# Kernel tuning notes

Measured on AMD Instinct MI355X. Metric: run time of the kernel, lower is better.

## Reference

```python
import jax, jax.numpy as jnp
import numpy as np

BS, OBS_LEN, TS, GW, GH = 1024, 8, 64, 32, 32
HID = 64          # hidden size of both LSTMs (hardcoded in __init__)
TEOM_IN = 36      # 6*6 flattened teom features (zeros in the original forward)


def setup_inputs() -> dict:
    key = jax.random.key(0)
    ks = jax.random.split(key, 22)
    r = lambda k, s, sc=0.1: jax.random.normal(k, s, dtype=jnp.float32) * sc
    return dict(
        obsv=r(ks[0], (BS, OBS_LEN, 2), 1.0),
        teom=jax.random.uniform(ks[1], (BS, TS, GW, GH), dtype=jnp.float32),
        # lstm_obsv (input 2 -> hidden 64), PyTorch gate order i,f,g,o
        Wih_o=r(ks[2], (4 * HID, 2)), Whh_o=r(ks[3], (4 * HID, HID)),
        bih_o=r(ks[4], (4 * HID,)), bhh_o=r(ks[5], (4 * HID,)),
        # lstm_teom (input 36 -> hidden 64)
        Wih_t=r(ks[6], (4 * HID, TEOM_IN)), Whh_t=r(ks[7], (4 * HID, HID)),
        bih_t=r(ks[8], (4 * HID,)), bhh_t=r(ks[9], (4 * HID,)),
        Wof=r(ks[10], (64, HID)), bof=r(ks[11], (64,)),
        Wtf=r(ks[12], (64, HID)), btf=r(ks[13], (64,)),
        Wmix=r(ks[14], (64, 128)), bmix=r(ks[15], (64,)),
        W1=r(ks[16], (32, 64)), b1=r(ks[17], (32,)),
        W2=r(ks[18], (32, 32)), b2=r(ks[19], (32,)),
        W3=r(ks[20], (2, 32)), b3=r(ks[21], (2,)),
    )


def _cell(x, h, c, Wih, Whh, b):
    # standard torch LSTMCell math; b = b_ih + b_hh
    g = x @ Wih.T + h @ Whh.T + b
    i, f, gg, o = jnp.split(g, 4, axis=-1)
    c_new = jax.nn.sigmoid(f) * c + jax.nn.sigmoid(i) * jnp.tanh(gg)
    h_new = jax.nn.sigmoid(o) * jnp.tanh(c_new)
    return h_new, c_new


def reference(obsv, teom, Wih_o, Whh_o, bih_o, bhh_o, Wih_t, Whh_t, bih_t, bhh_t,
              Wof, bof, Wtf, btf, Wmix, bmix, W1, b1, W2, b2, W3, b3):
    bs, out_len = teom.shape[0], teom.shape[1]
    dt = obsv.dtype
    b_o = bih_o + bhh_o
    b_t = bih_t + bhh_t
    # conved_teom_flat is hard zeros in the original forward (convs never called)
    z_teom = jnp.zeros((bs, Wih_t.shape[1]), dt)
    lrelu = lambda v: jnp.where(v >= 0, v, 0.1 * v)  # LeakyReLU(0.1)

    def mix_out(h_t, h_o, buf):
        # buf: [bs, 3, 2] = last three positions (obsv[:,-3:,:])
        ts_ = h_t @ Wtf.T + btf
        os_ = h_o @ Wof.T + bof
        m = jnp.concatenate([ts_, os_], axis=1) @ Wmix.T + bmix
        a = lrelu(m @ W1.T + b1)
        a = lrelu(a @ W2.T + b2)
        o = a @ W3.T + b3
        # y = out(y_mix) + obsv[:,-1,:] + (obsv[:,-1,:] - obsv[:,-3,:]) / 2
        return o + buf[:, -1] + (buf[:, -1] - buf[:, 0]) * 0.5

    h_o = jnp.zeros((bs, HID), dt); c_o = jnp.zeros((bs, HID), dt)
    h_t = jnp.zeros((bs, HID), dt); c_t = jnp.zeros((bs, HID), dt)

    # ---- t == 0: obsv LSTM consumes the full observed trajectory
    def obsv_scan(carry, x_t):
        h, c = carry
        h, c = _cell(x_t, h, c, Wih_o, Whh_o, b_o)
        return (h, c), None
    (h_o, c_o), _ = jax.lax.scan(obsv_scan, (h_o, c_o), obsv.transpose(1, 0, 2))
    h_t, c_t = _cell(z_teom, h_t, c_t, Wih_t, Whh_t, b_t)
    buf = obsv[:, -3:, :]
    y0 = mix_out(h_t, h_o, buf)
    buf = jnp.concatenate([buf[:, 1:], y0[:, None]], axis=1)

    # ---- t = 1 .. out_len-1: obsv LSTM steps on previous prediction
    def step(carry, _):
        h_o, c_o, h_t, c_t, buf = carry
        h_t, c_t = _cell(z_teom, h_t, c_t, Wih_t, Whh_t, b_t)
        h_o, c_o = _cell(buf[:, -1], h_o, c_o, Wih_o, Whh_o, b_o)
        y_t = mix_out(h_t, h_o, buf)
        buf = jnp.concatenate([buf[:, 1:], y_t[:, None]], axis=1)
        return (h_o, c_o, h_t, c_t, buf), y_t

    _, ys = jax.lax.scan(step, (h_o, c_o, h_t, c_t, buf), None, length=out_len - 1)
    y = jnp.concatenate([y0[:, None], ys.transpose(1, 0, 2)], axis=1)  # [bs, out_len, 2]
    # teom_cropped is all-zeros in the original forward -> c is exactly zeros
    c_out = jnp.zeros((bs, out_len), dt)
    return y, c_out
```

## Files before the change

### kernel.cpp

```cpp
#include <hip/hip_runtime.h>

#define BS 1024
#define TS 64

__device__ __forceinline__ float sigf(float x){ return 1.f/(1.f+__expf(-x)); }
__device__ __forceinline__ float tanh_fast(float x){
  float cx = fminf(fmaxf(x,-15.f),15.f);
  float e = __expf(2.f*cx);
  return (e-1.f)/(e+1.f);
}
__device__ __forceinline__ float lrelu(float v){ return v>=0.f ? v : 0.1f*v; }
__device__ __forceinline__ float dot4(float4 a, float4 b){
  return a.x*b.x + a.y*b.y + a.z*b.z + a.w*b.w;
}

__global__ __launch_bounds__(256) void precompute_kernel(
    const float* __restrict__ Whh_t, const float* __restrict__ bih_t,
    const float* __restrict__ bhh_t,
    const float* __restrict__ Wof,  const float* __restrict__ bof,
    const float* __restrict__ Wtf,  const float* __restrict__ btf,
    const float* __restrict__ Wmix, const float* __restrict__ bmix,
    float* __restrict__ ws_wcomb, float* __restrict__ ws_mbias)
{
  __shared__ __align__(16) float sHall[TS*64];
  __shared__ __align__(16) float sTs[TS*64];
  __shared__ float sWof[64*64];
  __shared__ float sG[256];
  __shared__ float sBof[64];
  __shared__ float sCmr[64];

  const int t = threadIdx.x;

  float4 wrow[16];
#pragma unroll
  for (int j=0;j<16;++j) wrow[j] = reinterpret_cast<const float4*>(Whh_t + t*64)[j];
  const float btr = bih_t[t] + bhh_t[t];

  for (int i=t;i<4096;i+=256) sWof[i] = Wof[i];
  if (t<64) sBof[t] = bof[t];
  __syncthreads();

  float c_reg = 0.f;
  for (int s=0;s<TS;++s){
    float a0=btr, a1=0.f, a2=0.f, a3=0.f;
    if (s>0){
      const float4* h4 = reinterpret_cast<const float4*>(sHall + (s-1)*64);
#pragma unroll
      for (int j=0;j<16;j+=4){
        a0 += dot4(wrow[j],   h4[j]);
        a1 += dot4(wrow[j+1], h4[j+1]);
        a2 += dot4(wrow[j+2], h4[j+2]);
        a3 += dot4(wrow[j+3], h4[j+3]);
      }
    }
    sG[t] = (a0+a1)+(a2+a3);
    __syncthreads();
    if (t<64){
      float gi=sG[t], gf=sG[64+t], gg=sG[128+t], go=sG[192+t];
      c_reg = sigf(gf)*c_reg + sigf(gi)*tanh_fast(gg);
      sHall[s*64+t] = sigf(go)*tanh_fast(c_reg);
    }
    __syncthreads();
  }

  if (t<64){
    float acc = bmix[t];
    for (int k=0;k<64;++k) acc += Wmix[t*128+64+k]*sBof[k];
    sCmr[t] = acc;
  }
  for (int o=t;o<TS*64;o+=256){
    int s=o>>6, i=o&63;
    float acc = btf[i];
    for (int k=0;k<64;++k) acc += Wtf[i*64+k]*sHall[s*64+k];
    sTs[o] = acc;
  }
  for (int o=t;o<4096;o+=256){
    int r=o>>6, j=o&63;
    float acc = 0.f;
    for (int k=0;k<64;++k) acc += Wmix[r*128+64+k]*sWof[k*64+j];
    ws_wcomb[o] = acc;
  }
  __syncthreads();
  for (int o=t;o<TS*64;o+=256){
    int s=o>>6, j=o&63;
    float acc = sCmr[j];
    for (int k=0;k<64;++k) acc += Wmix[j*128+k]*sTs[s*64+k];
    ws_mbias[o] = acc;
  }
}

__global__ __launch_bounds__(256, 4) void main_kernel(
    const float* __restrict__ obsv,
    const float* __restrict__ Wih_o, const float* __restrict__ Whh_o,
    const float* __restrict__ bih_o, const float* __restrict__ bhh_o,
    const float* __restrict__ W1, const float* __restrict__ b1,
    const float* __restrict__ W2, const float* __restrict__ b2,
    const float* __restrict__ W3, const float* __restrict__ b3,
    const float* __restrict__ wcomb, const float* __restrict__ mbias,
    float* __restrict__ out)
{
  __shared__ __align__(16) float4 sWc[16*64];
  __shared__ __align__(16) float4 sW1[16*32];
  __shared__ __align__(16) float4 sW2[8*32];
  __shared__ float sG[256];
  __shared__ __align__(16) float sHb[64];
  __shared__ __align__(16) float sM[64];
  __shared__ __align__(16) float sA1[32];
  __shared__ float sY[2];
  __shared__ float sObs[16];

  const int t    = threadIdx.x;
  const int blk  = blockIdx.x;
  const int lane = t & 63;
  const int w    = t >> 6;
  const int tw   = (blk + (blk >> 8)) & 3;
  const bool tailw = (w == tw);

  if (t < 64) out[BS*TS*2 + blk*64 + t] = 0.f;

  for (int i=t;i<1024;i+=256) sWc[i] = reinterpret_cast<const float4*>(wcomb)[(i&63)*16 + (i>>6)];
  for (int i=t;i<512;i+=256)  sW1[i] = reinterpret_cast<const float4*>(W1)[(i&31)*16 + (i>>5)];
  if (t<256)                  sW2[t] = reinterpret_cast<const float4*>(W2)[(t&31)*8 + (t>>5)];
  if (t<16) sObs[t] = obsv[blk*16 + t];
  if (t<64) sHb[t] = 0.f;

  float4 wrow[16];
#pragma unroll
  for (int j=0;j<16;++j) wrow[j] = reinterpret_cast<const float4*>(Whh_o + t*64)[j];
  const float wi0  = Wih_o[2*t];
  const float wi1  = Wih_o[2*t+1];
  const float b_or = bih_o[t] + bhh_o[t];

  const int rr = lane & 31, hf = lane >> 5;
  const float b1r = b1[rr], b2r = b2[rr];
  const float w30 = W3[rr], w31 = W3[32+rr];
  const float b30 = b3[0],  b31 = b3[1];
  float bl00=0,bl01=0,bl10=0,bl11=0,bl20=0,bl21=0;
  float c_reg = 0.f;

  __syncthreads();

  if (tailw){
    bl00 = sObs[10]; bl01 = sObs[11];
    bl10 = sObs[12]; bl11 = sObs[13];
    bl20 = sObs[14]; bl21 = sObs[15];
  }

  const float4* sH4   = reinterpret_cast<const float4*>(sHb);
  const float4* sM4   = reinterpret_cast<const float4*>(sM);
  const float4* sA14  = reinterpret_cast<const float4*>(sA1);

  for (int it=0; it<71; ++it){
    float mb = 0.f;
    if (tailw && it >= 7) mb = mbias[(it-7)*64 + lane];

    float x0, x1;
    if (it < 8){ x0 = sObs[2*it]; x1 = sObs[2*it+1]; }
    else       { x0 = sY[0];      x1 = sY[1]; }
    float a0 = b_or + wi0*x0 + wi1*x1, p0 = 0.f;
#pragma unroll
    for (int q=0;q<16;q+=2){
      a0 += dot4(wrow[q],   sH4[q]);
      p0 += dot4(wrow[q+1], sH4[q+1]);
    }
    sG[t] = a0 + p0;
    __syncthreads();

    if (tailw){
      __builtin_amdgcn_s_setprio(1);
      const float g0 = sG[lane],     g1 = sG[64+lane];
      const float g2 = sG[128+lane], g3 = sG[192+lane];
      c_reg = sigf(g1)*c_reg + sigf(g0)*tanh_fast(g2);
      const float h = sigf(g3)*tanh_fast(c_reg);
      sHb[lane] = h;
      __builtin_amdgcn_wave_barrier();

      if (it >= 7){
        float m0 = mb, m1 = 0.f, m2 = 0.f, m3 = 0.f;
#pragma unroll
        for (int q=0;q<16;q+=4){
          m0 += dot4(sWc[q*64+lane],     sH4[q]);
          m1 += dot4(sWc[(q+1)*64+lane], sH4[q+1]);
          m2 += dot4(sWc[(q+2)*64+lane], sH4[q+2]);
          m3 += dot4(sWc[(q+3)*64+lane], sH4[q+3]);
        }
        sM[lane] = (m0+m1)+(m2+m3);
        __builtin_amdgcn_wave_barrier();

        float u = 0.f;
#pragma unroll
        for (int q=0;q<8;++q) u += dot4(sW1[(hf*8+q)*32+rr], sM4[hf*8+q]);
        u += __shfl_xor(u, 32);
        if (lane < 32) sA1[lane] = lrelu(u + b1r);
        __builtin_amdgcn_wave_barrier();

        float v = 0.f;
#pragma unroll
        for (int q=0;q<4;++q) v += dot4(sW2[(hf*4+q)*32+rr], sA14[hf*4+q]);
        v += __shfl_xor(v, 32);
        const float a2v = lrelu(v + b2r);

        float q0 = a2v*w30, q1 = a2v*w31;
#pragma unroll
        for (int m=1;m<=16;m<<=1){
          q0 += __shfl_xor(q0, m);
          q1 += __shfl_xor(q1, m);
        }
        const float y0 = q0 + b30 + bl20 + (bl20 - bl00)*0.5f;
        const float y1 = q1 + b31 + bl21 + (bl21 - bl01)*0.5f;
        bl00 = bl10; bl01 = bl11;
        bl10 = bl20; bl11 = bl21;
        bl20 = y0;   bl21 = y1;
        if (lane == 0){
          sY[0] = y0; sY[1] = y1;
          *reinterpret_cast<float2*>(out + (size_t)(blk*TS + (it-7))*2)
              = make_float2(y0, y1);
        }
      }
      __builtin_amdgcn_s_setprio(0);
    }
    __syncthreads();
  }
}

extern "C" void kernel_launch(void* const* d_in, const int* in_sizes, int n_in,
                              void* d_out, int out_size, void* d_ws, size_t ws_size,
                              hipStream_t stream)
{
  const float* obsv  = (const float*)d_in[0];
  const float* Wih_o = (const float*)d_in[2];
  const float* Whh_o = (const float*)d_in[3];
  const float* bih_o = (const float*)d_in[4];
  const float* bhh_o = (const float*)d_in[5];
  const float* Whh_t = (const float*)d_in[7];
  const float* bih_t = (const float*)d_in[8];
  const float* bhh_t = (const float*)d_in[9];
  const float* Wof   = (const float*)d_in[10];
  const float* bof   = (const float*)d_in[11];
  const float* Wtf   = (const float*)d_in[12];
  const float* btf   = (const float*)d_in[13];
  const float* Wmix  = (const float*)d_in[14];
  const float* bmix  = (const float*)d_in[15];
  const float* W1    = (const float*)d_in[16];
  const float* b1    = (const float*)d_in[17];
  const float* W2    = (const float*)d_in[18];
  const float* b2    = (const float*)d_in[19];
  const float* W3    = (const float*)d_in[20];
  const float* b3    = (const float*)d_in[21];

  float* wsf = (float*)d_ws;

  precompute_kernel<<<1,256,0,stream>>>(Whh_t,bih_t,bhh_t,Wof,bof,Wtf,btf,
                                        Wmix,bmix, wsf, wsf+4096);
  main_kernel<<<BS,256,0,stream>>>(obsv,Wih_o,Whh_o,bih_o,bhh_o,
                                   W1,b1,W2,b2,W3,b3,
                                   wsf, wsf+4096,
                                   (float*)d_out);
}
```

Measured before the change: 614.3 us.

## Fold mix and W1 layers into precompute; redundant per-wave LSTM cell with 128 threads

The precompute kernel now multiplies W1 into the combined mix weight and bias, so the main kernel goes straight from h to the first MLP layer and drops one 64x64 matvec per step. The main kernel uses 128 threads, each computing two gate rows. Both waves redundantly compute the cell update and the MLP tail, so there is a single __syncthreads per step, with sG double-buffered. This trades duplicated elementwise work and more registers per thread for fewer block barriers and less serial matvec work on the critical path.

New measurement: 536.1 us. -12.7%, faster.

```diff
diff --git a/kernel.cpp b/kernel.cpp
--- a/kernel.cpp
+++ b/kernel.cpp
@@ -20,11 +20,14 @@
     const float* __restrict__ Wof,  const float* __restrict__ bof,
     const float* __restrict__ Wtf,  const float* __restrict__ btf,
     const float* __restrict__ Wmix, const float* __restrict__ bmix,
-    float* __restrict__ ws_wcomb, float* __restrict__ ws_mbias)
+    const float* __restrict__ W1,   const float* __restrict__ b1,
+    float* __restrict__ ws_wx, float* __restrict__ ws_mb1)
 {
   __shared__ __align__(16) float sHall[TS*64];
   __shared__ __align__(16) float sTs[TS*64];
   __shared__ float sWof[64*64];
+  __shared__ float sWcb[64*64];
+  __shared__ float sMb[TS*64];
   __shared__ float sG[256];
   __shared__ float sBof[64];
   __shared__ float sCmr[64];
@@ -78,148 +81,142 @@
     int r=o>>6, j=o&63;
     float acc = 0.f;
     for (int k=0;k<64;++k) acc += Wmix[r*128+64+k]*sWof[k*64+j];
-    ws_wcomb[o] = acc;
+    sWcb[o] = acc;
   }
   __syncthreads();
   for (int o=t;o<TS*64;o+=256){
     int s=o>>6, j=o&63;
     float acc = sCmr[j];
     for (int k=0;k<64;++k) acc += Wmix[j*128+k]*sTs[s*64+k];
-    ws_mbias[o] = acc;
-  }
-}
-
-__global__ __launch_bounds__(256, 4) void main_kernel(
+    sMb[o] = acc;
+  }
+  __syncthreads();
+  for (int o=t;o<32*64;o+=256){
+    int r=o>>6, j=o&63;
+    float acc = 0.f;
+    for (int k=0;k<64;++k) acc += W1[r*64+k]*sWcb[k*64+j];
+    ws_wx[o] = acc;
+  }
+  for (int o=t;o<TS*32;o+=256){
+    int s=o>>5, r=o&31;
+    float acc = b1[r];
+    for (int k=0;k<64;++k) acc += W1[r*64+k]*sMb[s*64+k];
+    ws_mb1[o] = acc;
+  }
+}
+
+__global__ __launch_bounds__(128, 2) void main_kernel(
     const float* __restrict__ obsv,
     const float* __restrict__ Wih_o, const float* __restrict__ Whh_o,
     const float* __restrict__ bih_o, const float* __restrict__ bhh_o,
-    const float* __restrict__ W1, const float* __restrict__ b1,
     const float* __restrict__ W2, const float* __restrict__ b2,
     const float* __restrict__ W3, const float* __restrict__ b3,
-    const float* __restrict__ wcomb, const float* __restrict__ mbias,
+    const float* __restrict__ wx, const float* __restrict__ mb1,
     float* __restrict__ out)
 {
-  __shared__ __align__(16) float4 sWc[16*64];
-  __shared__ __align__(16) float4 sW1[16*32];
+  __shared__ __align__(16) float4 sWx[16*32];
   __shared__ __align__(16) float4 sW2[8*32];
-  __shared__ float sG[256];
-  __shared__ __align__(16) float sHb[64];
-  __shared__ __align__(16) float sM[64];
-  __shared__ __align__(16) float sA1[32];
-  __shared__ float sY[2];
+  __shared__ float sG[2][256];
+  __shared__ __align__(16) float sHb[2][64];
+  __shared__ __align__(16) float sA1[2][32];
   __shared__ float sObs[16];
 
   const int t    = threadIdx.x;
   const int blk  = blockIdx.x;
   const int lane = t & 63;
   const int w    = t >> 6;
-  const int tw   = (blk + (blk >> 8)) & 3;
-  const bool tailw = (w == tw);
 
   if (t < 64) out[BS*TS*2 + blk*64 + t] = 0.f;
 
-  for (int i=t;i<1024;i+=256) sWc[i] = reinterpret_cast<const float4*>(wcomb)[(i&63)*16 + (i>>6)];
-  for (int i=t;i<512;i+=256)  sW1[i] = reinterpret_cast<const float4*>(W1)[(i&31)*16 + (i>>5)];
-  if (t<256)                  sW2[t] = reinterpret_cast<const float4*>(W2)[(t&31)*8 + (t>>5)];
+  for (int i=t;i<512;i+=128) sWx[i] = reinterpret_cast<const float4*>(wx)[(i&31)*16 + (i>>5)];
+  for (int i=t;i<256;i+=128) sW2[i] = reinterpret_cast<const float4*>(W2)[(i&31)*8 + (i>>5)];
   if (t<16) sObs[t] = obsv[blk*16 + t];
-  if (t<64) sHb[t] = 0.f;
-
-  float4 wrow[16];
-#pragma unroll
-  for (int j=0;j<16;++j) wrow[j] = reinterpret_cast<const float4*>(Whh_o + t*64)[j];
-  const float wi0  = Wih_o[2*t];
-  const float wi1  = Wih_o[2*t+1];
-  const float b_or = bih_o[t] + bhh_o[t];
+  sHb[t>>6][t&63] = 0.f;
+
+  const int r0 = w*128 + lane, r1 = r0 + 64;
+  float4 wr0[16], wr1[16];
+#pragma unroll
+  for (int j=0;j<16;++j){
+    wr0[j] = reinterpret_cast<const float4*>(Whh_o + r0*64)[j];
+    wr1[j] = reinterpret_cast<const float4*>(Whh_o + r1*64)[j];
+  }
+  const float wi00 = Wih_o[2*r0], wi01 = Wih_o[2*r0+1];
+  const float wi10 = Wih_o[2*r1], wi11 = Wih_o[2*r1+1];
+  const float bR0 = bih_o[r0] + bhh_o[r0];
+  const float bR1 = bih_o[r1] + bhh_o[r1];
 
   const int rr = lane & 31, hf = lane >> 5;
-  const float b1r = b1[rr], b2r = b2[rr];
+  const float b2r = b2[rr];
   const float w30 = W3[rr], w31 = W3[32+rr];
   const float b30 = b3[0],  b31 = b3[1];
-  float bl00=0,bl01=0,bl10=0,bl11=0,bl20=0,bl21=0;
-  float c_reg = 0.f;
-
-  __syncthreads();
-
-  if (tailw){
-    bl00 = sObs[10]; bl01 = sObs[11];
-    bl10 = sObs[12]; bl11 = sObs[13];
-    bl20 = sObs[14]; bl21 = sObs[15];
-  }
-
-  const float4* sH4   = reinterpret_cast<const float4*>(sHb);
-  const float4* sM4   = reinterpret_cast<const float4*>(sM);
-  const float4* sA14  = reinterpret_cast<const float4*>(sA1);
+
+  __syncthreads();
+
+  float bl00 = sObs[10], bl01 = sObs[11];
+  float bl10 = sObs[12], bl11 = sObs[13];
+  float bl20 = sObs[14], bl21 = sObs[15];
+  float c_reg = 0.f, y0r = 0.f, y1r = 0.f;
+
+  const float4* sH4w  = reinterpret_cast<const float4*>(sHb[w]);
+  const float4* sA14w = reinterpret_cast<const float4*>(sA1[w]);
 
   for (int it=0; it<71; ++it){
     float mb = 0.f;
-    if (tailw && it >= 7) mb = mbias[(it-7)*64 + lane];
+    if (it >= 7) mb = mb1[(it-7)*32 + rr];
 
     float x0, x1;
     if (it < 8){ x0 = sObs[2*it]; x1 = sObs[2*it+1]; }
-    else       { x0 = sY[0];      x1 = sY[1]; }
-    float a0 = b_or + wi0*x0 + wi1*x1, p0 = 0.f;
+    else       { x0 = y0r;        x1 = y1r; }
+    float a0 = bR0 + wi00*x0 + wi01*x1, p0 = 0.f;
+    float a1 = bR1 + wi10*x0 + wi11*x1, p1 = 0.f;
 #pragma unroll
     for (int q=0;q<16;q+=2){
-      a0 += dot4(wrow[q],   sH4[q]);
-      p0 += dot4(wrow[q+1], sH4[q+1]);
-    }
-    sG[t] = a0 + p0;
+      const float4 h0 = sH4w[q], h1 = sH4w[q+1];
+      a0 += dot4(wr0[q],h0);  p0 += dot4(wr0[q+1],h1);
+      a1 += dot4(wr1[q],h0);  p1 += dot4(wr1[q+1],h1);
+    }
+    const int pb = it & 1;
+    sG[pb][r0] = a0 + p0;
+    sG[pb][r1] = a1 + p1;
     __syncthreads();
 
-    if (tailw){
-      __builtin_amdgcn_s_setprio(1);
-      const float g0 = sG[lane],     g1 = sG[64+lane];
-      const float g2 = sG[128+lane], g3 = sG[192+lane];
-      c_reg = sigf(g1)*c_reg + sigf(g0)*tanh_fast(g2);
-      const float h = sigf(g3)*tanh_fast(c_reg);
-      sHb[lane] = h;
+    const float g0 = sG[pb][lane],     g1 = sG[pb][64+lane];
+    const float g2 = sG[pb][128+lane], g3 = sG[pb][192+lane];
+    c_reg = sigf(g1)*c_reg + sigf(g0)*tanh_fast(g2);
+    const float h = sigf(g3)*tanh_fast(c_reg);
+    sHb[w][lane] = h;
+    __builtin_amdgcn_wave_barrier();
+
+    if (it >= 7){
+      float u = 0.f;
+#pragma unroll
+      for (int q=0;q<8;++q) u += dot4(sWx[(hf*8+q)*32+rr], sH4w[hf*8+q]);
+      u += __shfl_xor(u, 32);
+      if (lane < 32) sA1[w][lane] = lrelu(u + mb);
       __builtin_amdgcn_wave_barrier();
 
-      if (it >= 7){
-        float m0 = mb, m1 = 0.f, m2 = 0.f, m3 = 0.f;
-#pragma unroll
-        for (int q=0;q<16;q+=4){
-          m0 += dot4(sWc[q*64+lane],     sH4[q]);
-          m1 += dot4(sWc[(q+1)*64+lane], sH4[q+1]);
-          m2 += dot4(sWc[(q+2)*64+lane], sH4[q+2]);
-          m3 += dot4(sWc[(q+3)*64+lane], sH4[q+3]);
-        }
-        sM[lane] = (m0+m1)+(m2+m3);
-        __builtin_amdgcn_wave_barrier();
-
-        float u = 0.f;
-#pragma unroll
-        for (int q=0;q<8;++q) u += dot4(sW1[(hf*8+q)*32+rr], sM4[hf*8+q]);
-        u += __shfl_xor(u, 32);
-        if (lane < 32) sA1[lane] = lrelu(u + b1r);
-        __builtin_amdgcn_wave_barrier();
-
-        float v = 0.f;
-#pragma unroll
-        for (int q=0;q<4;++q) v += dot4(sW2[(hf*4+q)*32+rr], sA14[hf*4+q]);
-        v += __shfl_xor(v, 32);
-        const float a2v = lrelu(v + b2r);
-
-        float q0 = a2v*w30, q1 = a2v*w31;
-#pragma unroll
-        for (int m=1;m<=16;m<<=1){
-          q0 += __shfl_xor(q0, m);
-          q1 += __shfl_xor(q1, m);
-        }
-        const float y0 = q0 + b30 + bl20 + (bl20 - bl00)*0.5f;
-        const float y1 = q1 + b31 + bl21 + (bl21 - bl01)*0.5f;
-        bl00 = bl10; bl01 = bl11;
-        bl10 = bl20; bl11 = bl21;
-        bl20 = y0;   bl21 = y1;
-        if (lane == 0){
-          sY[0] = y0; sY[1] = y1;
-          *reinterpret_cast<float2*>(out + (size_t)(blk*TS + (it-7))*2)
-              = make_float2(y0, y1);
-        }
+      float v = 0.f;
+#pragma unroll
+      for (int q=0;q<4;++q) v += dot4(sW2[(hf*4+q)*32+rr], sA14w[hf*4+q]);
+      v += __shfl_xor(v, 32);
+      const float a2v = lrelu(v + b2r);
+
+      float q0 = a2v*w30, q1 = a2v*w31;
+#pragma unroll
+      for (int m=1;m<=16;m<<=1){
+        q0 += __shfl_xor(q0, m);
+        q1 += __shfl_xor(q1, m);
       }
-      __builtin_amdgcn_s_setprio(0);
-    }
-    __syncthreads();
+      const float y0 = q0 + b30 + bl20 + (bl20 - bl00)*0.5f;
+      const float y1 = q1 + b31 + bl21 + (bl21 - bl01)*0.5f;
+      bl00 = bl10; bl01 = bl11;
+      bl10 = bl20; bl11 = bl21;
+      bl20 = y0;   bl21 = y1;
+      y0r = y0;    y1r = y1;
+      if (w == 0 && lane == 0)
+        *reinterpret_cast<float2*>(out + (size_t)(blk*TS + (it-7))*2)
+            = make_float2(y0, y1);
+    }
   }
 }
 
@@ -251,9 +248,9 @@
   float* wsf = (float*)d_ws;
 
   precompute_kernel<<<1,256,0,stream>>>(Whh_t,bih_t,bhh_t,Wof,bof,Wtf,btf,
-                                        Wmix,bmix, wsf, wsf+4096);
-  main_kernel<<<BS,256,0,stream>>>(obsv,Wih_o,Whh_o,bih_o,bhh_o,
-                                   W1,b1,W2,b2,W3,b3,
-                                   wsf, wsf+4096,
+                                        Wmix,bmix, W1,b1, wsf, wsf+2048);
+  main_kernel<<<BS,128,0,stream>>>(obsv,Wih_o,Whh_o,bih_o,bhh_o,
+                                   W2,b2,W3,b3,
+                                   wsf, wsf+2048,
                                    (float*)d_out);
 }
```
